# Performance work log

Hardware: AMD Instinct MI355X
Metric: run time of the kernel (lower is better)

## Reference

```python
import jax, jax.numpy as jnp
import numpy as np

EPS = 1e-5

def _ln(x, g, b):
    m = x.mean(-1, keepdims=True)
    v = jnp.var(x, axis=-1, keepdims=True)
    return (x - m) * jax.lax.rsqrt(v + EPS) * g + b

def _conv(x, w, b, stride=1, pad=1):
    y = jax.lax.conv_general_dilated(x, w, (stride, stride), [(pad, pad), (pad, pad)],
                                     dimension_numbers=('NCHW', 'OIHW', 'NCHW'))
    return y + b[None, :, None, None]

def _bn(x, g, b, m, v):
    # inference-mode BatchNorm2d
    inv = jax.lax.rsqrt(v + EPS)
    return (x - m[None, :, None, None]) * (g * inv)[None, :, None, None] + b[None, :, None, None]

def _sru_dir(u0, u1, u2, res, vf, vr, bf, br, reverse):
    # elementwise gated recurrence (SRU v2, identity activation, no dropout)
    def step(c, inp):
        a0, a1, a2, rx = inp
        f = jax.nn.sigmoid(a1 + vf * c + bf)
        c2 = f * c + (1.0 - f) * a0
        r = jax.nn.sigmoid(a2 + vr * c2 + br)
        return c2, r * c2 + (1.0 - r) * rx
    c0 = jnp.zeros_like(u0[0])
    _, hs = jax.lax.scan(step, c0, (u0, u1, u2, res), reverse=reverse)
    return hs

def _sru_layer(x, g, b, wp, w, vc, bias, k, h):
    # x: [L,B,n_in]; layer_norm on input, factored weight (projection), bidirectional
    xn = _ln(x, g, b)
    L, B, _ = xn.shape
    U = (xn @ wp) @ w                      # [L,B,2*k*h]
    U = U.reshape(L, B, 2, k, h)
    outs = []
    for d, rev in ((0, False), (1, True)):
        u = U[:, :, d]
        res = u[..., 3, :] if k == 4 else xn[..., d * h:(d + 1) * h]
        outs.append(_sru_dir(u[..., 0, :], u[..., 1, :], u[..., 2, :], res,
                             vc[d, 0], vc[d, 1], bias[d, 0], bias[d, 1], rev))
    return jnp.concatenate(outs, axis=-1)

def _forward(x, conv0_w, conv0_b, rconv1_w, rconv1_b, rbn1_g, rbn1_b, rbn1_m, rbn1_v,
             rconv2_w, rconv2_b, rbn2_g, rbn2_b, rbn2_m, rbn2_v,
             ln0_g, ln0_b, wproj0, w0, vc0, bias0, ln_g, ln_b, wproj, w, vc, bias,
             cln_g, cln_b, cls_w):
    H = 512
    h = _conv(x, conv0_w, conv0_b, stride=2)           # [B,32,F/2,T/2]
    for i in range(3):                                  # 3 residual blocks
        r = h
        h1 = jax.nn.relu(_bn(_conv(h, rconv1_w[i], rconv1_b[i]), rbn1_g[i], rbn1_b[i], rbn1_m[i], rbn1_v[i]))
        h2 = _bn(_conv(h1, rconv2_w[i], rconv2_b[i]), rbn2_g[i], rbn2_b[i], rbn2_m[i], rbn2_v[i])
        h = jax.nn.relu(h2 + r)
    Bb, C, Fr, Tt = h.shape
    s = h.reshape(Bb, C * Fr, Tt).transpose(2, 0, 1)   # [T,B,2048]
    s = _sru_layer(s, ln0_g, ln0_b, wproj0, w0, vc0, bias0, 4, H)  # layer 0: n_in != n_out -> k=4
    for i in range(3):                                  # layers 1..3: n_in == n_out -> k=3
        s = _sru_layer(s, ln_g[i], ln_b[i], wproj[i], w[i], vc[i], bias[i], 3, H)
    s = s.transpose(1, 0, 2)                            # [B,T,1024]
    s = _ln(s, cln_g, cln_b)
    return s @ cls_w                                    # [B,T,30]

def setup_inputs():
    key = jax.random.key(0)
    ks = iter(jax.random.split(key, 32))
    def nrm(shape, scale=1.0):
        return jax.random.normal(next(ks), shape, jnp.float32) * scale
    H, P, F2, D, hb = 512, 256, 2048, 1024, -2.0
    d = {}
    d['x'] = nrm((16, 1, 128, 2048))
    d['conv0_w'] = nrm((32, 1, 3, 3), (2.0 / 9) ** 0.5)
    d['conv0_b'] = jnp.zeros((32,))
    d['rconv1_w'] = nrm((3, 32, 32, 3, 3), (2.0 / (32 * 9)) ** 0.5)
    d['rconv1_b'] = jnp.zeros((3, 32))
    d['rbn1_g'] = jnp.ones((3, 32)); d['rbn1_b'] = jnp.zeros((3, 32))
    d['rbn1_m'] = nrm((3, 32), 0.1); d['rbn1_v'] = jnp.ones((3, 32))
    d['rconv2_w'] = nrm((3, 32, 32, 3, 3), (2.0 / (32 * 9)) ** 0.5)
    d['rconv2_b'] = jnp.zeros((3, 32))
    d['rbn2_g'] = 0.1 * jnp.ones((3, 32)); d['rbn2_b'] = jnp.zeros((3, 32))
    d['rbn2_m'] = nrm((3, 32), 0.1); d['rbn2_v'] = jnp.ones((3, 32))
    d['ln0_g'] = jnp.ones((F2,)); d['ln0_b'] = jnp.zeros((F2,))
    d['wproj0'] = nrm((F2, P), F2 ** -0.5)
    d['w0'] = nrm((P, 2 * 4 * H), P ** -0.5)
    d['vc0'] = nrm((2, 2, H), 0.1)
    d['bias0'] = jnp.zeros((2, 2, H)).at[:, 0].set(hb)
    d['ln_g'] = jnp.ones((3, D)); d['ln_b'] = jnp.zeros((3, D))
    d['wproj'] = nrm((3, D, P), D ** -0.5)
    d['w'] = nrm((3, P, 2 * 3 * H), P ** -0.5)
    d['vc'] = nrm((3, 2, 2, H), 0.1)
    d['bias'] = jnp.zeros((3, 2, 2, H)).at[:, :, 0].set(hb)
    d['cln_g'] = jnp.ones((D,)); d['cln_b'] = jnp.zeros((D,))
    d['cls_w'] = nrm((D, 30), D ** -0.5)
    return d

def reference(x, conv0_w, conv0_b, rconv1_w, rconv1_b, rbn1_g, rbn1_b, rbn1_m, rbn1_v,
              rconv2_w, rconv2_b, rbn2_g, rbn2_b, rbn2_m, rbn2_v,
              ln0_g, ln0_b, wproj0, w0, vc0, bias0, ln_g, ln_b, wproj, w, vc, bias,
              cln_g, cln_b, cls_w):
    return _forward(x, conv0_w, conv0_b, rconv1_w, rconv1_b, rbn1_g, rbn1_b, rbn1_m, rbn1_v,
                    rconv2_w, rconv2_b, rbn2_g, rbn2_b, rbn2_m, rbn2_v,
                    ln0_g, ln0_b, wproj0, w0, vc0, bias0, ln_g, ln_b, wproj, w, vc, bias,
                    cln_g, cln_b, cls_w)
```

## Files before the change

kernel.cpp:

```cpp
#include <hip/hip_runtime.h>
#include <hip/hip_bf16.h>
#include <math.h>

#define DEV __device__ __forceinline__

typedef __attribute__((ext_vector_type(8))) short short8;
typedef __attribute__((ext_vector_type(4))) float floatx4;

DEV float b2f_lo(unsigned u) { return __uint_as_float(u << 16); }
DEV float b2f_hi(unsigned u) { return __uint_as_float(u & 0xffff0000u); }

#if __has_builtin(__builtin_amdgcn_exp2f)
DEV float fexp2_(float x) { return __builtin_amdgcn_exp2f(x); }
#else
DEV float fexp2_(float x) { return exp2f(x); }
#endif
#if __has_builtin(__builtin_amdgcn_rcpf)
DEV float frcp_(float x) { return __builtin_amdgcn_rcpf(x); }
#else
DEV float frcp_(float x) { return 1.f / x; }
#endif

DEV void gl2lds16(const void* g, void* l) {
  __builtin_amdgcn_global_load_lds(
      (const __attribute__((address_space(1))) unsigned int*)g,
      (__attribute__((address_space(3))) unsigned int*)l, 16, 0, 0);
}

union U8 { uint4 u; __hip_bfloat16 h[8]; };

DEV int swz64(int x)    { return (x & ~63) | ((x & 15) << 2) | ((x >> 4) & 3); }
DEV int invswz64(int x) { return (x & ~63) | ((x & 3) << 4) | ((x >> 2) & 15); }

__global__ __launch_bounds__(256) void conv_stem_nhwc(const float* __restrict__ x,
    const float* __restrict__ w, const float* __restrict__ bias,
    __hip_bfloat16* __restrict__ out) {
  __shared__ float sX[3][2052];
  __shared__ float sW[288];
  __shared__ float sB[32];
  const int tid = threadIdx.x;
  const int f = blockIdx.x, n = blockIdx.y;
  const float* xb = x + (size_t)n * 262144;

  for (int i = tid; i < 1536; i += 256) {
    int r = i >> 9, c4 = i & 511;
    int fi = 2 * f - 1 + r;
    float4 v = {0.f, 0.f, 0.f, 0.f};
    if (fi >= 0 && fi < 128) v = *(const float4*)&xb[fi * 2048 + c4 * 4];
    sX[r][1 + c4 * 4 + 0] = v.x;
    sX[r][1 + c4 * 4 + 1] = v.y;
    sX[r][1 + c4 * 4 + 2] = v.z;
    sX[r][1 + c4 * 4 + 3] = v.w;
  }
  if (tid < 3) { sX[tid][0] = 0.f; sX[tid][2049] = 0.f; }
  for (int i = tid; i < 288; i += 256) sW[i] = w[i];
  if (tid < 32) sB[tid] = bias[tid];
  __syncthreads();

  float xv[4][9];
#pragma unroll
  for (int q = 0; q < 4; ++q) {
    int t = tid + q * 256;
#pragma unroll
    for (int r = 0; r < 3; ++r)
#pragma unroll
      for (int dc = 0; dc < 3; ++dc)
        xv[q][r * 3 + dc] = sX[r][2 * t + dc];
  }

  U8 ores[4][4];
#pragma unroll
  for (int ocq = 0; ocq < 4; ++ocq) {
#pragma unroll
    for (int oo = 0; oo < 8; ++oo) {
      float w9[9];
#pragma unroll
      for (int qq = 0; qq < 9; ++qq) w9[qq] = sW[(ocq * 8 + oo) * 9 + qq];
      float b0 = sB[ocq * 8 + oo];
#pragma unroll
      for (int q = 0; q < 4; ++q) {
        float acc = b0;
#pragma unroll
        for (int qq = 0; qq < 9; ++qq) acc = fmaf(w9[qq], xv[q][qq], acc);
        ores[ocq][q].h[oo] = __float2bfloat16(acc);
      }
    }
  }

#pragma unroll
  for (int q = 0; q < 4; ++q) {
    int t = tid + q * 256;
    uint4* dst = (uint4*)&out[(((size_t)n * 64 + f) * 1024 + t) * 32];
    dst[0] = ores[0][q].u;
    dst[1] = ores[1][q].u;
    dst[2] = ores[2][q].u;
    dst[3] = ores[3][q].u;
  }
}

__global__ __launch_bounds__(256) void wtap_conv6(const float* __restrict__ w1,
    const float* __restrict__ w2, __hip_bfloat16* __restrict__ out) {
  int i = blockIdx.x * 256 + threadIdx.x;
  if (i < 55296) {
    int b = i / 9216, r = i - b * 9216;
    int layer = b >> 1, which = b & 1;
    const float* src = (which ? w2 : w1) + layer * 9216;
    int tap = r >> 10, oc = (r >> 5) & 31, ic = r & 31;
    out[b * 9216 + r] = __float2bfloat16(src[(oc * 32 + ic) * 9 + tap]);
  }
}

template <int ADD>
__global__ __launch_bounds__(256) void conv_mfma(const __hip_bfloat16* __restrict__ Hin,
    const __hip_bfloat16* __restrict__ wt,
    const float* __restrict__ cb, const float* __restrict__ bg,
    const float* __restrict__ bb, const float* __restrict__ bm,
    const float* __restrict__ bv, __hip_bfloat16* Hres) {
  __shared__ __hip_bfloat16 sIn[6 * 66 * 40];
  __hip_bfloat16* sOut = sIn;
  const int tid = threadIdx.x;
  const int tb = blockIdx.x, fb = blockIdx.y, n = blockIdx.z;
  const int t0 = tb * 64, f0 = fb * 4;
  const __hip_bfloat16* Hb = Hin + (size_t)n * 2097152;

  for (int c = tid; c < 1584; c += 256) {
    int rr = c / 264;
    int r2 = c - rr * 264;
    int p = r2 >> 2, icq = r2 & 3;
    int fi = f0 - 1 + rr;
    int tg = t0 + p - 1;
    uint4 v = {0, 0, 0, 0};
    if (fi >= 0 && fi < 64 && tg >= 0 && tg < 1024)
      v = *(const uint4*)&Hb[((size_t)fi * 1024 + tg) * 32 + icq * 8];
    *(uint4*)&sIn[(rr * 66 + p) * 40 + icq * 8] = v;
  }

  const int lane = tid & 63, wave = tid >> 6;
  const int fr = lane & 15, fq = lane >> 4;
  short8 bfrag[9][2];
#pragma unroll
  for (int tap = 0; tap < 9; ++tap)
#pragma unroll
    for (int j = 0; j < 2; ++j)
      bfrag[tap][j] = *(const short8*)&wt[(tap * 32 + j * 16 + fr) * 32 + fq * 8];

  __syncthreads();

  const int tw = wave * 16;
  floatx4 acc[4][2];
#pragma unroll
  for (int fp = 0; fp < 4; ++fp)
#pragma unroll
    for (int j = 0; j < 2; ++j) acc[fp][j] = (floatx4){0.f, 0.f, 0.f, 0.f};

#pragma unroll
  for (int fp = 0; fp < 4; ++fp) {
    int pbase = tw + fr;
#pragma unroll
    for (int df = 0; df < 3; ++df)
#pragma unroll
      for (int dc = 0; dc < 3; ++dc) {
        short8 af =
            *(const short8*)&sIn[((fp + df) * 66 + pbase + dc) * 40 + fq * 8];
        acc[fp][0] = __builtin_amdgcn_mfma_f32_16x16x32_bf16(
            af, bfrag[df * 3 + dc][0], acc[fp][0], 0, 0, 0);
        acc[fp][1] = __builtin_amdgcn_mfma_f32_16x16x32_bf16(
            af, bfrag[df * 3 + dc][1], acc[fp][1], 0, 0, 0);
      }
  }

  float sc0 = bg[fr] * rsqrtf(bv[fr] + 1e-5f);
  float sh0 = (cb[fr] - bm[fr]) * sc0 + bb[fr];
  float sc1 = bg[fr + 16] * rsqrtf(bv[fr + 16] + 1e-5f);
  float sh1 = (cb[fr + 16] - bm[fr + 16]) * sc1 + bb[fr + 16];

  __syncthreads();
#pragma unroll
  for (int fp = 0; fp < 4; ++fp)
#pragma unroll
    for (int j = 0; j < 2; ++j) {
      float sc = j ? sc1 : sc0, sh = j ? sh1 : sh0;
#pragma unroll
      for (int reg = 0; reg < 4; ++reg) {
        int t_l = tw + fq * 4 + reg;
        sOut[(fp * 64 + t_l) * 40 + j * 16 + fr] =
            __float2bfloat16(acc[fp][j][reg] * sc + sh);
      }
    }
  __syncthreads();

  for (int c = tid; c < 1024; c += 256) {
    int fp = c >> 8, rem = c & 255;
    int t_l = rem >> 2, icq = rem & 3;
    U8 y;
    y.u = *(uint4*)&sOut[(fp * 64 + t_l) * 40 + icq * 8];
    size_t addr = (((size_t)n * 64 + f0 + fp) * 1024 + t0 + t_l) * 32 + icq * 8;
    U8 o;
    if (ADD) {
      U8 r;
      r.u = *(const uint4*)&Hres[addr];
#pragma unroll
      for (int i = 0; i < 8; ++i)
        o.h[i] = __float2bfloat16(
            fmaxf(__bfloat162float(y.h[i]) + __bfloat162float(r.h[i]), 0.f));
    } else {
#pragma unroll
      for (int i = 0; i < 8; ++i)
        o.h[i] = __float2bfloat16(fmaxf(__bfloat162float(y.h[i]), 0.f));
    }
    *(uint4*)&Hres[addr] = o.u;
  }
}

__global__ __launch_bounds__(256) void ln_nhwc(const __hip_bfloat16* __restrict__ H,
    const float* __restrict__ g, const float* __restrict__ b,
    __hip_bfloat16* __restrict__ xn) {
  int r = blockIdx.x;
  int t = r >> 4, n = r & 15;
  int tid = threadIdx.x;
  int f = tid >> 2, icq = tid & 3;
  U8 v;
  v.u = *(const uint4*)&H[(((size_t)n * 64 + f) * 1024 + t) * 32 + icq * 8];
  float xv[8];
  float sum = 0.f, ss = 0.f;
#pragma unroll
  for (int i = 0; i < 8; ++i) {
    xv[i] = __bfloat162float(v.h[i]);
    sum += xv[i];
    ss += xv[i] * xv[i];
  }
#pragma unroll
  for (int off = 32; off > 0; off >>= 1) {
    sum += __shfl_down(sum, off);
    ss  += __shfl_down(ss, off);
  }
  __shared__ float red[8];
  int lane = tid & 63, wave = tid >> 6;
  if (lane == 0) { red[wave] = sum; red[4 + wave] = ss; }
  __syncthreads();
  sum = red[0] + red[1] + red[2] + red[3];
  ss  = red[4] + red[5] + red[6] + red[7];
  float mean = sum * (1.f / 2048.f);
  float var = ss * (1.f / 2048.f) - mean * mean;
  float inv = rsqrtf(var + 1e-5f);
  U8 o;
#pragma unroll
  for (int i = 0; i < 8; ++i) {
    int cf = (icq * 8 + i) * 64 + f;
    o.h[i] = __float2bfloat16((xv[i] - mean) * inv * g[cf] + b[cf]);
  }
  *(uint4*)&xn[(size_t)r * 2048 + tid * 8] = o.u;
}

__global__ __launch_bounds__(256) void wt_perm0(const float* __restrict__ in,
    __hip_bfloat16* __restrict__ out) {
  int i = blockIdx.x * 256 + threadIdx.x;
  int p = i >> 11, kp = i & 2047;
  int ic = kp & 31, f = kp >> 5;
  out[i] = __float2bfloat16(in[(ic * 64 + f) * 256 + p]);
}

__global__ __launch_bounds__(256) void wt_bf16(const float* __restrict__ in,
    __hip_bfloat16* __restrict__ out, int K, int N, int inStride, int outStride) {
  __shared__ float tile[32][33];
  int x = threadIdx.x, y0 = threadIdx.y;
  int bn = blockIdx.x * 32;
  int bk = blockIdx.y * 32;
  const float* src = in + (size_t)blockIdx.z * inStride;
  __hip_bfloat16* dst = out + (size_t)blockIdx.z * outStride;
#pragma unroll
  for (int i = 0; i < 4; ++i) {
    int yy = y0 + i * 8;
    tile[yy][x] = src[(size_t)(bk + yy) * N + bn + x];
  }
  __syncthreads();
#pragma unroll
  for (int i = 0; i < 4; ++i) {
    int yy = y0 + i * 8;
    dst[(size_t)(bn + yy) * K + bk + x] = __float2bfloat16(tile[x][yy]);
  }
}

__global__ void wexp_prep(const float* __restrict__ in,
    __hip_bfloat16* __restrict__ out, int korig, int inStride, int outStride) {
  __shared__ float tile[32][33];
  int jt = blockIdx.x;
  int ckt = blockIdx.y;
  int z = blockIdx.z;
  int layer = z >> 3, dk = z & 7;
  int d = dk >> 2, k = dk & 3;
  if (k >= korig) return;
  const float* src = in + (size_t)layer * inStride;
  __hip_bfloat16* dst = out + (size_t)layer * outStride;
  int x = threadIdx.x, y0 = threadIdx.y;
#pragma unroll
  for (int i = 0; i < 4; ++i) {
    int yy = y0 + i * 8;
    tile[yy][x] = src[(size_t)(ckt * 32 + yy) * (korig * 1024) +
                      (d * korig + k) * 512 + jt * 32 + x];
  }
  __syncthreads();
#pragma unroll
  for (int i = 0; i < 4; ++i) {
    int yy = y0 + i * 8;
    int ch = d * 512 + jt * 32 + yy;
    int rOld;
    if (korig == 4)
      rOld = (k < 2) ? (ch * 2 + k) : (2048 + ch * 2 + (k - 2));
    else
      rOld = (k < 2) ? (ch * 2 + k) : (2048 + ch);
    int rNew = invswz64(rOld);
    int ckp = swz64(ckt * 32 + x);
    dst[(size_t)rNew * 256 + ckp] = __float2bfloat16(tile[x][yy]);
  }
}

__global__ __launch_bounds__(256) void colsb_prep(const float* __restrict__ bias0,
    const float* __restrict__ bias3, float2* __restrict__ out) {
  int i = blockIdx.x * 256 + threadIdx.x;
  if (i >= 13312) return;
  const float NL2E = -1.44269504f;
  float s = 1.f, bb = 0.f;
  if (i < 4096) {
    int col = i;
    if (col < 2048) {
      int ch = col >> 1, e = col & 1;
      int d = ch >> 9, jj = ch & 511;
      if (e) { s = NL2E; bb = NL2E * bias0[d * 1024 + jj]; }
    } else {
      int cc = col - 2048, ch = cc >> 1, e = cc & 1;
      int d = ch >> 9, jj = ch & 511;
      if (!e) { s = NL2E; bb = NL2E * bias0[d * 1024 + 512 + jj]; }
    }
  } else {
    int rem = i - 4096;
    int layer = rem / 3072, col = rem - layer * 3072;
    const float* bsrc = bias3 + layer * 2048;
    if (col < 2048) {
      int ch = col >> 1, e = col & 1;
      int d = ch >> 9, jj = ch & 511;
      if (e) { s = NL2E; bb = NL2E * bsrc[d * 1024 + jj]; }
    } else {
      int ch = col - 2048;
      int d = ch >> 9, jj = ch & 511;
      s = NL2E; bb = NL2E * bsrc[d * 1024 + 512 + jj];
    }
  }
  out[i] = make_float2(s, bb);
}

__global__ __launch_bounds__(256) void wct_prep(const float* __restrict__ in,
    __hip_bfloat16* __restrict__ out) {
  int i = blockIdx.x * 256 + threadIdx.x;
  int nn = i >> 10, kk = i & 1023;
  out[i] = __float2bfloat16(nn < 30 ? in[kk * 30 + nn] : 0.f);
}

__global__ __launch_bounds__(256) void gemm_bf16(const __hip_bfloat16* __restrict__ A,
    const __hip_bfloat16* __restrict__ Bt, __hip_bfloat16* __restrict__ C,
    const float2* __restrict__ csb, int M, int N, int K) {
  __shared__ __hip_bfloat16 As[2][128 * 64];
  __shared__ __hip_bfloat16 Bs[2][128 * 64];
  const int tid = threadIdx.x;
  const int gx = gridDim.x;
  const int nwg = gx * gridDim.y;
  const int bid = blockIdx.y * gx + blockIdx.x;
  const int wgid = (bid & 7) * (nwg >> 3) + (bid >> 3);
  const int m0 = (wgid / gx) * 128, n0 = (wgid % gx) * 128;
  const int lane = tid & 63, wave = tid >> 6;
  const int wm = wave & 1, wn = wave >> 1;
  const int fr = lane & 15, fq = lane >> 4;
  const int frx = fr & 7;

  const int srow8 = lane >> 3;
  const int lslot = (lane & 7) ^ srow8;
  const __hip_bfloat16* gaS = &A[(size_t)(m0 + wave * 32 + srow8) * K + lslot * 8];
  const __hip_bfloat16* gbS = &Bt[(size_t)(n0 + wave * 32 + srow8) * K + lslot * 8];

  floatx4 acc[4][4];
#pragma unroll
  for (int i = 0; i < 4; ++i)
#pragma unroll
    for (int j = 0; j < 4; ++j)
      acc[i][j] = (floatx4){0.f, 0.f, 0.f, 0.f};

#define STAGE(BUF, kk)                                                    \
  {                                                                       \
    _Pragma("unroll") for (int i = 0; i < 4; ++i) {                       \
      gl2lds16(gaS + (size_t)i * 8 * K + (kk),                            \
               &As[BUF][(wave * 32 + i * 8) * 64]);                       \
      gl2lds16(gbS + (size_t)i * 8 * K + (kk),                            \
               &Bs[BUF][(wave * 32 + i * 8) * 64]);                       \
    }                                                                     \
  }
#define COMPUTE(BUF)                                                      \
  {                                                                       \
    _Pragma("unroll") for (int s = 0; s < 2; ++s) {                       \
      const int sl = ((s * 4 + fq) ^ frx) * 8;                            \
      short8 af[4], bf_[4];                                               \
      _Pragma("unroll") for (int i = 0; i < 4; ++i) {                     \
        af[i]  = *(const short8*)&As[BUF][(wm * 64 + i * 16 + fr) * 64 + sl]; \
        bf_[i] = *(const short8*)&Bs[BUF][(wn * 64 + i * 16 + fr) * 64 + sl]; \
      }                                                                   \
      _Pragma("unroll") for (int i = 0; i < 4; ++i)                       \
        _Pragma("unroll") for (int j = 0; j < 4; ++j)                     \
          acc[i][j] = __builtin_amdgcn_mfma_f32_16x16x32_bf16(            \
              af[i], bf_[j], acc[i][j], 0, 0, 0);                         \
    }                                                                     \
  }
#define CFENCE asm volatile("" ::: "memory")

  STAGE(0, 0);
  for (int k0 = 0; k0 < K; k0 += 128) {
    STAGE(1, k0 + 64);
    asm volatile("s_waitcnt vmcnt(8)" ::: "memory");
    __builtin_amdgcn_s_barrier();
    COMPUTE(0);
    CFENCE;
    __builtin_amdgcn_s_barrier();
    if (k0 + 128 < K) {
      STAGE(0, k0 + 128);
      asm volatile("s_waitcnt vmcnt(8)" ::: "memory");
    } else {
      asm volatile("s_waitcnt vmcnt(0)" ::: "memory");
    }
    __builtin_amdgcn_s_barrier();
    COMPUTE(1);
    CFENCE;
    __builtin_amdgcn_s_barrier();
  }
#undef STAGE
#undef COMPUTE
#undef CFENCE

  const int p0 = n0 + wn * 64 + fr * 4;
  float s0 = 1.f, s1 = 1.f, s2 = 1.f, s3 = 1.f;
  float c0 = 0.f, c1 = 0.f, c2v = 0.f, c3 = 0.f;
  if (csb) {
    float2 t0 = csb[p0], t1 = csb[p0 + 1], t2 = csb[p0 + 2], t3 = csb[p0 + 3];
    s0 = t0.x; c0 = t0.y; s1 = t1.x; c1 = t1.y;
    s2 = t2.x; c2v = t2.y; s3 = t3.x; c3 = t3.y;
  }
#pragma unroll
  for (int i = 0; i < 4; ++i)
#pragma unroll
    for (int reg = 0; reg < 4; ++reg) {
      int row = m0 + wm * 64 + i * 16 + fq * 4 + reg;
      union { uint2 u; __hip_bfloat16 h[4]; } o;
      o.h[0] = __float2bfloat16(fmaf(acc[i][0][reg], s0, c0));
      o.h[1] = __float2bfloat16(fmaf(acc[i][1][reg], s1, c1));
      o.h[2] = __float2bfloat16(fmaf(acc[i][2][reg], s2, c2v));
      o.h[3] = __float2bfloat16(fmaf(acc[i][3][reg], s3, c3));
      *(uint2*)&C[(size_t)row * N + p0] = o.u;
    }
}

__global__ __launch_bounds__(256) void cls_gemm(const __hip_bfloat16* __restrict__ A,
    const __hip_bfloat16* __restrict__ Wct, float* __restrict__ out) {
  const int tid = threadIdx.x;
  const int lane = tid & 63, wave = tid >> 6;
  const int fr = lane & 15, fq = lane >> 4;
  const int m0 = (blockIdx.x * 4 + wave) * 16;
  floatx4 acc[2];
  acc[0] = (floatx4){0.f, 0.f, 0.f, 0.f};
  acc[1] = (floatx4){0.f, 0.f, 0.f, 0.f};
#pragma unroll 4
  for (int k0 = 0; k0 < 1024; k0 += 32) {
    short8 af = *(const short8*)&A[(size_t)(m0 + fr) * 1024 + k0 + fq * 8];
    short8 b0 = *(const short8*)&Wct[(size_t)fr * 1024 + k0 + fq * 8];
    short8 b1 = *(const short8*)&Wct[(size_t)(16 + fr) * 1024 + k0 + fq * 8];
    acc[0] = __builtin_amdgcn_mfma_f32_16x16x32_bf16(af, b0, acc[0], 0, 0, 0);
    acc[1] = __builtin_amdgcn_mfma_f32_16x16x32_bf16(af, b1, acc[1], 0, 0, 0);
  }
#pragma unroll
  for (int j = 0; j < 2; ++j) {
    int col = j * 16 + fr;
    if (col < 30) {
#pragma unroll
      for (int reg = 0; reg < 4; ++reg) {
        int row = m0 + fq * 4 + reg;
        int t = row >> 4, n = row & 15;
        out[(size_t)n * 30720 + t * 30 + col] = acc[j][reg];
      }
    }
  }
}

template <int ROWB>
__global__ __launch_bounds__(64) void scan_c(const __hip_bfloat16* __restrict__ U,
    const float* __restrict__ vc, __hip_bfloat16* __restrict__ c2out) {
  int gid = blockIdx.x * 64 + threadIdx.x;
  int j = gid & 511;
  int n = (gid >> 9) & 15;
  int d = gid >> 13;
  const float NL2E = -1.44269504f;
  float vf2 = NL2E * vc[d * 1024 + j];

  const char* Ub = (const char*)U + (size_t)n * ROWB + (size_t)(d * 512 + j) * 4;
  char* Ob = (char*)c2out + (size_t)n * 2048 + (size_t)(d * 512 + j) * 2;
  const int US = d ? -(16 * ROWB) : (16 * ROWB);
  const int OS = d ? -32768 : 32768;
  int uoff = d ? 1023 * 16 * ROWB : 0;
  int ooff = d ? 1023 * 32768 : 0;

  uint B0[16], B1[16], B2[16], B3[16];
  float c = 0.f;

#define LOADC(UB)                                                         \
  {                                                                       \
    _Pragma("unroll") for (int ss = 0; ss < 16; ++ss) {                   \
      UB[ss] = *(const uint*)(Ub + uoff);                                 \
      uoff += US;                                                         \
    }                                                                     \
  }

#define COMPC(UB)                                                         \
  {                                                                       \
    _Pragma("unroll") for (int ss = 0; ss < 16; ++ss) {                   \
      uint u = UB[ss];                                                    \
      float a0 = b2f_lo(u), a1p = b2f_hi(u);                              \
      float f = frcp_(1.f + fexp2_(fmaf(vf2, c, a1p)));                   \
      c = fmaf(f, c - a0, a0);                                            \
      *(__hip_bfloat16*)(Ob + ooff) = __float2bfloat16(c);                \
      ooff += OS;                                                         \
    }                                                                     \
  }

  LOADC(B0);
  LOADC(B1);
  LOADC(B2);
  for (int cb = 0; cb < 64; cb += 4) {
    LOADC(B3);
    COMPC(B0);
    if (cb + 4 < 64) LOADC(B0);
    COMPC(B1);
    if (cb + 5 < 64) LOADC(B1);
    COMPC(B2);
    if (cb + 6 < 64) LOADC(B2);
    COMPC(B3);
  }
#undef LOADC
#undef COMPC
}

template <int K4>
__global__ __launch_bounds__(256) void yln(const __hip_bfloat16* __restrict__ c2buf,
    const __hip_bfloat16* __restrict__ U, const __hip_bfloat16* __restrict__ xn,
    const float* __restrict__ vc, const float* __restrict__ g,
    const float* __restrict__ b, __hip_bfloat16* __restrict__ outx) {
  int r = blockIdx.x;
  int tid = threadIdx.x;
  int ch0 = tid * 4;
  const float NL2E = -1.44269504f;

  union { ushort4 u; __hip_bfloat16 h[4]; } cv;
  cv.u = *(const ushort4*)&c2buf[(size_t)r * 1024 + ch0];
  float a2p[4], rx[4];
  if (K4) {
    uint4 pr = *(const uint4*)((const char*)U + (size_t)r * 8192 + 4096 + tid * 16);
    uint pp[4] = {pr.x, pr.y, pr.z, pr.w};
#pragma unroll
    for (int i = 0; i < 4; ++i) { a2p[i] = b2f_lo(pp[i]); rx[i] = b2f_hi(pp[i]); }
  } else {
    union { ushort4 u; __hip_bfloat16 h[4]; } av, xv;
    av.u = *(const ushort4*)((const char*)U + (size_t)r * 6144 + 4096 + tid * 8);
    xv.u = *(const ushort4*)&xn[(size_t)r * 1024 + ch0];
#pragma unroll
    for (int i = 0; i < 4; ++i) {
      a2p[i] = __bfloat162float(av.h[i]);
      rx[i]  = __bfloat162float(xv.h[i]);
    }
  }

  int d = ch0 >> 9, j0 = ch0 & 511;
  float y[4], sum = 0.f, ss = 0.f;
#pragma unroll
  for (int i = 0; i < 4; ++i) {
    float vr2 = NL2E * vc[d * 1024 + 512 + j0 + i];
    float cc = __bfloat162float(cv.h[i]);
    float rr = frcp_(1.f + fexp2_(fmaf(vr2, cc, a2p[i])));
    y[i] = fmaf(rr, cc - rx[i], rx[i]);
    sum += y[i];
    ss += y[i] * y[i];
  }
#pragma unroll
  for (int off = 32; off > 0; off >>= 1) {
    sum += __shfl_down(sum, off);
    ss  += __shfl_down(ss, off);
  }
  __shared__ float red[8];
  int lane = tid & 63, wave = tid >> 6;
  if (lane == 0) { red[wave] = sum; red[4 + wave] = ss; }
  __syncthreads();
  sum = red[0] + red[1] + red[2] + red[3];
  ss  = red[4] + red[5] + red[6] + red[7];
  float mean = sum * (1.f / 1024.f);
  float var = ss * (1.f / 1024.f) - mean * mean;
  float inv = rsqrtf(var + 1e-5f);
  float4 gv = *(const float4*)&g[ch0];
  float4 bv = *(const float4*)&b[ch0];
  float gg[4] = {gv.x, gv.y, gv.z, gv.w};
  float bb[4] = {bv.x, bv.y, bv.z, bv.w};
  union { ushort4 u; __hip_bfloat16 h[4]; } o;
#pragma unroll
  for (int i = 0; i < 4; ++i)
    o.h[i] = __float2bfloat16((y[i] - mean) * inv * gg[i] + bb[i]);
  *(ushort4*)&outx[(size_t)r * 1024 + ch0] = o.u;
}

extern "C" void kernel_launch(void* const* d_in, const int* in_sizes, int n_in,
                              void* d_out, int out_size, void* d_ws, size_t ws_size,
                              hipStream_t stream) {
  const float* x        = (const float*)d_in[0];
  const float* conv0_w  = (const float*)d_in[1];
  const float* conv0_b  = (const float*)d_in[2];
  const float* rconv1_w = (const float*)d_in[3];
  const float* rconv1_b = (const float*)d_in[4];
  const float* rbn1_g   = (const float*)d_in[5];
  const float* rbn1_b   = (const float*)d_in[6];
  const float* rbn1_m   = (const float*)d_in[7];
  const float* rbn1_v   = (const float*)d_in[8];
  const float* rconv2_w = (const float*)d_in[9];
  const float* rconv2_b = (const float*)d_in[10];
  const float* rbn2_g   = (const float*)d_in[11];
  const float* rbn2_b   = (const float*)d_in[12];
  const float* rbn2_m   = (const float*)d_in[13];
  const float* rbn2_v   = (const float*)d_in[14];
  const float* ln0_g    = (const float*)d_in[15];
  const float* ln0_b    = (const float*)d_in[16];
  const float* wproj0   = (const float*)d_in[17];
  const float* w0       = (const float*)d_in[18];
  const float* vc0      = (const float*)d_in[19];
  const float* bias0    = (const float*)d_in[20];
  const float* ln_g     = (const float*)d_in[21];
  const float* ln_b     = (const float*)d_in[22];
  const float* wproj    = (const float*)d_in[23];
  const float* w        = (const float*)d_in[24];
  const float* vc       = (const float*)d_in[25];
  const float* bias     = (const float*)d_in[26];
  const float* cln_g    = (const float*)d_in[27];
  const float* cln_b    = (const float*)d_in[28];
  const float* cls_w    = (const float*)d_in[29];
  float* out = (float*)d_out;

  float* Af = (float*)d_ws;
  float* Bf = Af + 33554432;
  __hip_bfloat16* Ah = (__hip_bfloat16*)Af;
  __hip_bfloat16* Bh = (__hip_bfloat16*)Bf;

  __hip_bfloat16* hA     = Ah;
  __hip_bfloat16* hB     = Bh;
  __hip_bfloat16* wt_all = Ah + 62914560;
  __hip_bfloat16* Wp0t   = Ah + 52428800;

  __hip_bfloat16* c2   = Bh;
  __hip_bfloat16* xnc  = Bh + 16777216;
  __hip_bfloat16* xn3  = Bh + 33554432;
  __hip_bfloat16* tmp  = Bh + 50331648;
  __hip_bfloat16* W3p  = Bh + 54525952;
  __hip_bfloat16* W0p  = Bh + 57671680;
  __hip_bfloat16* Wpt3 = Bh + 58720256;
  float2* csb          = (float2*)(Bh + 59506688);
  __hip_bfloat16* xn0  = Bh;
  __hip_bfloat16* U    = Ah;
  __hip_bfloat16* Wct  = Ah;

  const float2* csb4 = csb;
  const float2* csb3 = csb + 4096;

  wtap_conv6<<<216, 256, 0, stream>>>(rconv1_w, rconv2_w, wt_all);
  wt_perm0<<<2048, 256, 0, stream>>>(wproj0, Wp0t);
  wexp_prep<<<dim3(16, 8, 8), dim3(32, 8), 0, stream>>>(w0, W0p, 4, 0, 0);
  wexp_prep<<<dim3(16, 8, 24), dim3(32, 8), 0, stream>>>(w, W3p, 3,
                                                         786432, 786432);
  wt_bf16<<<dim3(8, 32, 3), dim3(32, 8), 0, stream>>>(wproj, Wpt3, 1024, 256,
                                                      262144, 262144);
  colsb_prep<<<52, 256, 0, stream>>>(bias0, bias, csb);

  conv_stem_nhwc<<<dim3(64, 16), 256, 0, stream>>>(x, conv0_w, conv0_b, hA);
  for (int i = 0; i < 3; ++i) {
    conv_mfma<0><<<dim3(16, 16, 16), 256, 0, stream>>>(hA, wt_all + (i * 2) * 9216,
        rconv1_b + i * 32, rbn1_g + i * 32, rbn1_b + i * 32,
        rbn1_m + i * 32, rbn1_v + i * 32, hB);
    conv_mfma<1><<<dim3(16, 16, 16), 256, 0, stream>>>(hB, wt_all + (i * 2 + 1) * 9216,
        rconv2_b + i * 32, rbn2_g + i * 32, rbn2_b + i * 32,
        rbn2_m + i * 32, rbn2_v + i * 32, hA);
  }

  ln_nhwc<<<16384, 256, 0, stream>>>(hA, ln0_g, ln0_b, xn0);
  gemm_bf16<<<dim3(2, 128), 256, 0, stream>>>(xn0, Wp0t, tmp, nullptr,
                                              16384, 256, 2048);
  gemm_bf16<<<dim3(32, 128), 256, 0, stream>>>(tmp, W0p, U, csb4,
                                               16384, 4096, 256);
  scan_c<8192><<<256, 64, 0, stream>>>(U, vc0, c2);
  __hip_bfloat16* xnA = xn3;
  __hip_bfloat16* xnB = xnc;
  yln<1><<<16384, 256, 0, stream>>>(c2, U, nullptr, vc0, ln_g, ln_b, xnA);

  for (int i = 0; i < 3; ++i) {
    gemm_bf16<<<dim3(2, 128), 256, 0, stream>>>(xnA, Wpt3 + i * 262144, tmp,
                                                nullptr, 16384, 256, 1024);
    gemm_bf16<<<dim3(24, 128), 256, 0, stream>>>(tmp, W3p + i * 786432, U,
                                                 csb3 + i * 3072, 16384, 3072, 256);
    scan_c<6144><<<256, 64, 0, stream>>>(U, vc + i * 2048, c2);
    const float* gg = (i < 2) ? (ln_g + (i + 1) * 1024) : cln_g;
    const float* bb = (i < 2) ? (ln_b + (i + 1) * 1024) : cln_b;
    yln<0><<<16384, 256, 0, stream>>>(c2, U, xnA, vc + i * 2048, gg, bb, xnB);
    __hip_bfloat16* sw = xnA; xnA = xnB; xnB = sw;
  }

  wct_prep<<<128, 256, 0, stream>>>(cls_w, Wct);
  cls_gemm<<<256, 256, 0, stream>>>(xnA, Wct, out);
}
```

Measured before the change: 974.7 us.

## Split GEMM epilogue into time-major scan buffer and separate gate/residual buffer

The second projection GEMM now writes its output in two layouts. The (a0,a1) pairs go to a channel-major buffer where each channel's 16 batch elements are contiguous per timestep. The remaining columns go to a compact separate buffer. The scan kernel is remapped so each 16-lane group reads one channel across 16 batch entries contiguously, making its strided serial loads coalesced. yln reads the smaller compact buffer. The cost is a more scattered store pattern in the GEMM epilogue.

```diff
diff --git a/kernel.cpp b/kernel.cpp
--- a/kernel.cpp
+++ b/kernel.cpp
@@ -356,8 +356,10 @@
   out[i] = __float2bfloat16(nn < 30 ? in[kk * 30 + nn] : 0.f);
 }
 
+template <int SPLIT>
 __global__ __launch_bounds__(256) void gemm_bf16(const __hip_bfloat16* __restrict__ A,
     const __hip_bfloat16* __restrict__ Bt, __hip_bfloat16* __restrict__ C,
+    uint* __restrict__ U01, __hip_bfloat16* __restrict__ U23,
     const float2* __restrict__ csb, int M, int N, int K) {
   __shared__ __hip_bfloat16 As[2][128 * 64];
   __shared__ __hip_bfloat16 Bs[2][128 * 64];
@@ -441,18 +443,56 @@
     s0 = t0.x; c0 = t0.y; s1 = t1.x; c1 = t1.y;
     s2 = t2.x; c2v = t2.y; s3 = t3.x; c3 = t3.y;
   }
-#pragma unroll
-  for (int i = 0; i < 4; ++i)
-#pragma unroll
-    for (int reg = 0; reg < 4; ++reg) {
-      int row = m0 + wm * 64 + i * 16 + fq * 4 + reg;
-      union { uint2 u; __hip_bfloat16 h[4]; } o;
-      o.h[0] = __float2bfloat16(fmaf(acc[i][0][reg], s0, c0));
-      o.h[1] = __float2bfloat16(fmaf(acc[i][1][reg], s1, c1));
-      o.h[2] = __float2bfloat16(fmaf(acc[i][2][reg], s2, c2v));
-      o.h[3] = __float2bfloat16(fmaf(acc[i][3][reg], s3, c3));
-      *(uint2*)&C[(size_t)row * N + p0] = o.u;
-    }
+
+  if (SPLIT == 0) {
+#pragma unroll
+    for (int i = 0; i < 4; ++i)
+#pragma unroll
+      for (int reg = 0; reg < 4; ++reg) {
+        int row = m0 + wm * 64 + i * 16 + fq * 4 + reg;
+        union { uint2 u; __hip_bfloat16 h[4]; } o;
+        o.h[0] = __float2bfloat16(fmaf(acc[i][0][reg], s0, c0));
+        o.h[1] = __float2bfloat16(fmaf(acc[i][1][reg], s1, c1));
+        o.h[2] = __float2bfloat16(fmaf(acc[i][2][reg], s2, c2v));
+        o.h[3] = __float2bfloat16(fmaf(acc[i][3][reg], s3, c3));
+        *(uint2*)&C[(size_t)row * N + p0] = o.u;
+      }
+  } else if (p0 < 2048) {
+    const int cell0 = p0 >> 1;
+    uint4* ub = (uint4*)U01;
+#pragma unroll
+    for (int i = 0; i < 4; ++i) {
+      int t = (m0 + wm * 64 + i * 16) >> 4;
+      union { uint4 u; __hip_bfloat16 h[8]; } q0, q1;
+#pragma unroll
+      for (int reg = 0; reg < 4; ++reg) {
+        q0.h[reg * 2]     = __float2bfloat16(fmaf(acc[i][0][reg], s0, c0));
+        q0.h[reg * 2 + 1] = __float2bfloat16(fmaf(acc[i][1][reg], s1, c1));
+        q1.h[reg * 2]     = __float2bfloat16(fmaf(acc[i][2][reg], s2, c2v));
+        q1.h[reg * 2 + 1] = __float2bfloat16(fmaf(acc[i][3][reg], s3, c3));
+      }
+      ub[((size_t)cell0 * 1024 + t) * 4 + fq] = q0.u;
+      ub[((size_t)(cell0 + 1) * 1024 + t) * 4 + fq] = q1.u;
+    }
+  } else {
+    const int cc = p0 - 2048;
+#pragma unroll
+    for (int i = 0; i < 4; ++i)
+#pragma unroll
+      for (int reg = 0; reg < 4; ++reg) {
+        int row = m0 + wm * 64 + i * 16 + fq * 4 + reg;
+        union { uint2 u; __hip_bfloat16 h[4]; } o;
+        o.h[0] = __float2bfloat16(fmaf(acc[i][0][reg], s0, c0));
+        o.h[1] = __float2bfloat16(fmaf(acc[i][1][reg], s1, c1));
+        o.h[2] = __float2bfloat16(fmaf(acc[i][2][reg], s2, c2v));
+        o.h[3] = __float2bfloat16(fmaf(acc[i][3][reg], s3, c3));
+        if (SPLIT == 1) {
+          *(uint2*)&((uint*)U23)[(size_t)row * 1024 + (cc >> 1)] = o.u;
+        } else {
+          *(uint2*)&U23[(size_t)row * 1024 + cc] = o.u;
+        }
+      }
+  }
 }
 
 __global__ __launch_bounds__(256) void cls_gemm(const __hip_bfloat16* __restrict__ A,
@@ -486,21 +526,21 @@
   }
 }
 
-template <int ROWB>
-__global__ __launch_bounds__(64) void scan_c(const __hip_bfloat16* __restrict__ U,
+__global__ __launch_bounds__(64) void scan_c(const uint* __restrict__ U01,
     const float* __restrict__ vc, __hip_bfloat16* __restrict__ c2out) {
-  int gid = blockIdx.x * 64 + threadIdx.x;
-  int j = gid & 511;
-  int n = (gid >> 9) & 15;
-  int d = gid >> 13;
+  int b = blockIdx.x;
+  int lane = threadIdx.x;
+  int ch = (b & 31) * 32 + (b >> 5) * 4 + (lane >> 4);
+  int n = lane & 15;
+  int d = ch >> 9;
   const float NL2E = -1.44269504f;
-  float vf2 = NL2E * vc[d * 1024 + j];
-
-  const char* Ub = (const char*)U + (size_t)n * ROWB + (size_t)(d * 512 + j) * 4;
-  char* Ob = (char*)c2out + (size_t)n * 2048 + (size_t)(d * 512 + j) * 2;
-  const int US = d ? -(16 * ROWB) : (16 * ROWB);
+  float vf2 = NL2E * vc[d * 1024 + (ch & 511)];
+
+  const uint* Up = U01 + (size_t)ch * 16384 + n;
+  char* Ob = (char*)c2out + ((size_t)n * 1024 + ch) * 2;
+  const int US = d ? -16 : 16;
   const int OS = d ? -32768 : 32768;
-  int uoff = d ? 1023 * 16 * ROWB : 0;
+  int uoff = d ? 1023 * 16 : 0;
   int ooff = d ? 1023 * 32768 : 0;
 
   uint B0[16], B1[16], B2[16], B3[16];
@@ -509,7 +549,7 @@
 #define LOADC(UB)                                                         \
   {                                                                       \
     _Pragma("unroll") for (int ss = 0; ss < 16; ++ss) {                   \
-      UB[ss] = *(const uint*)(Ub + uoff);                                 \
+      UB[ss] = Up[uoff];                                                  \
       uoff += US;                                                         \
     }                                                                     \
   }
@@ -545,7 +585,7 @@
 
 template <int K4>
 __global__ __launch_bounds__(256) void yln(const __hip_bfloat16* __restrict__ c2buf,
-    const __hip_bfloat16* __restrict__ U, const __hip_bfloat16* __restrict__ xn,
+    const __hip_bfloat16* __restrict__ U23, const __hip_bfloat16* __restrict__ xn,
     const float* __restrict__ vc, const float* __restrict__ g,
     const float* __restrict__ b, __hip_bfloat16* __restrict__ outx) {
   int r = blockIdx.x;
@@ -557,13 +597,13 @@
   cv.u = *(const ushort4*)&c2buf[(size_t)r * 1024 + ch0];
   float a2p[4], rx[4];
   if (K4) {
-    uint4 pr = *(const uint4*)((const char*)U + (size_t)r * 8192 + 4096 + tid * 16);
+    uint4 pr = *(const uint4*)((const char*)U23 + (size_t)r * 4096 + tid * 16);
     uint pp[4] = {pr.x, pr.y, pr.z, pr.w};
 #pragma unroll
     for (int i = 0; i < 4; ++i) { a2p[i] = b2f_lo(pp[i]); rx[i] = b2f_hi(pp[i]); }
   } else {
     union { ushort4 u; __hip_bfloat16 h[4]; } av, xv;
-    av.u = *(const ushort4*)((const char*)U + (size_t)r * 6144 + 4096 + tid * 8);
+    av.u = *(const ushort4*)((const char*)U23 + (size_t)r * 2048 + tid * 8);
     xv.u = *(const ushort4*)&xn[(size_t)r * 1024 + ch0];
 #pragma unroll
     for (int i = 0; i < 4; ++i) {
@@ -653,6 +693,10 @@
   __hip_bfloat16* wt_all = Ah + 62914560;
   __hip_bfloat16* Wp0t   = Ah + 52428800;
 
+  uint* U01            = (uint*)Ah;
+  __hip_bfloat16* U23  = Ah + 33554432;
+  __hip_bfloat16* Wct  = Ah;
+
   __hip_bfloat16* c2   = Bh;
   __hip_bfloat16* xnc  = Bh + 16777216;
   __hip_bfloat16* xn3  = Bh + 33554432;
@@ -662,8 +706,6 @@
   __hip_bfloat16* Wpt3 = Bh + 58720256;
   float2* csb          = (float2*)(Bh + 59506688);
   __hip_bfloat16* xn0  = Bh;
-  __hip_bfloat16* U    = Ah;
-  __hip_bfloat16* Wct  = Ah;
 
   const float2* csb4 = csb;
   const float2* csb3 = csb + 4096;
@@ -688,24 +730,26 @@
   }
 
   ln_nhwc<<<16384, 256, 0, stream>>>(hA, ln0_g, ln0_b, xn0);
-  gemm_bf16<<<dim3(2, 128), 256, 0, stream>>>(xn0, Wp0t, tmp, nullptr,
-                                              16384, 256, 2048);
-  gemm_bf16<<<dim3(32, 128), 256, 0, stream>>>(tmp, W0p, U, csb4,
-                                               16384, 4096, 256);
-  scan_c<8192><<<256, 64, 0, stream>>>(U, vc0, c2);
+  gemm_bf16<0><<<dim3(2, 128), 256, 0, stream>>>(xn0, Wp0t, tmp, nullptr, nullptr,
+                                                 nullptr, 16384, 256, 2048);
+  gemm_bf16<1><<<dim3(32, 128), 256, 0, stream>>>(tmp, W0p, nullptr, U01, U23,
+                                                  csb4, 16384, 4096, 256);
+  scan_c<<<256, 64, 0, stream>>>(U01, vc0, c2);
   __hip_bfloat16* xnA = xn3;
   __hip_bfloat16* xnB = xnc;
-  yln<1><<<16384, 256, 0, stream>>>(c2, U, nullptr, vc0, ln_g, ln_b, xnA);
+  yln<1><<<16384, 256, 0, stream>>>(c2, U23, nullptr, vc0, ln_g, ln_b, xnA);
 
   for (int i = 0; i < 3; ++i) {
-    gemm_bf16<<<dim3(2, 128), 256, 0, stream>>>(xnA, Wpt3 + i * 262144, tmp,
-                                                nullptr, 16384, 256, 1024);
-    gemm_bf16<<<dim3(24, 128), 256, 0, stream>>>(tmp, W3p + i * 786432, U,
-                                                 csb3 + i * 3072, 16384, 3072, 256);
-    scan_c<6144><<<256, 64, 0, stream>>>(U, vc + i * 2048, c2);
+    gemm_bf16<0><<<dim3(2, 128), 256, 0, stream>>>(xnA, Wpt3 + i * 262144, tmp,
+                                                   nullptr, nullptr, nullptr,
+                                                   16384, 256, 1024);
+    gemm_bf16<2><<<dim3(24, 128), 256, 0, stream>>>(tmp, W3p + i * 786432, nullptr,
+                                                    U01, U23, csb3 + i * 3072,
+                                                    16384, 3072, 256);
+    scan_c<<<256, 64, 0, stream>>>(U01, vc + i * 2048, c2);
     const float* gg = (i < 2) ? (ln_g + (i + 1) * 1024) : cln_g;
     const float* bb = (i < 2) ? (ln_b + (i + 1) * 1024) : cln_b;
-    yln<0><<<16384, 256, 0, stream>>>(c2, U, xnA, vc + i * 2048, gg, bb, xnB);
+    yln<0><<<16384, 256, 0, stream>>>(c2, U23, xnA, vc + i * 2048, gg, bb, xnB);
     __hip_bfloat16* sw = xnA; xnA = xnB; xnB = sw;
   }
 
```

After: 1.010 ms. 3.6% more time.

## Warp-specialize SRU scan with a producer wave streaming U into an LDS ring

Applied to the files above, without the earlier changes.

The recurrent scan kernel now uses two waves per block. One producer wave issues async global-to-LDS loads of U into a 16-slot ring buffer, staying 12 blocks ahead of the consumer. The consumer wave reads gate inputs from LDS and runs the recurrence, with the two waves synchronised by block barriers. The aim is to hide global memory latency on the serial scan better than the register-based prefetch did, at the cost of 64KB of LDS per block and a barrier on every 16-step chunk.

```diff
diff --git a/kernel.cpp b/kernel.cpp
--- a/kernel.cpp
+++ b/kernel.cpp
@@ -487,60 +487,68 @@
 }
 
 template <int ROWB>
-__global__ __launch_bounds__(64) void scan_c(const __hip_bfloat16* __restrict__ U,
+__global__ __launch_bounds__(128) void scan_c(const __hip_bfloat16* __restrict__ U,
     const float* __restrict__ vc, __hip_bfloat16* __restrict__ c2out) {
-  int gid = blockIdx.x * 64 + threadIdx.x;
-  int j = gid & 511;
-  int n = (gid >> 9) & 15;
-  int d = gid >> 13;
+  __shared__ uint slab[16 * 1024];
+  const int b = blockIdx.x;
+  const int lane = threadIdx.x & 63;
+  const int wave = threadIdx.x >> 6;
+  const int jb = (b * 64) & 511;
+  const int n = (b >> 3) & 15;
+  const int d = b >> 7;
   const float NL2E = -1.44269504f;
-  float vf2 = NL2E * vc[d * 1024 + j];
-
-  const char* Ub = (const char*)U + (size_t)n * ROWB + (size_t)(d * 512 + j) * 4;
-  char* Ob = (char*)c2out + (size_t)n * 2048 + (size_t)(d * 512 + j) * 2;
-  const int US = d ? -(16 * ROWB) : (16 * ROWB);
-  const int OS = d ? -32768 : 32768;
-  int uoff = d ? 1023 * 16 * ROWB : 0;
-  int ooff = d ? 1023 * 32768 : 0;
-
-  uint B0[16], B1[16], B2[16], B3[16];
-  float c = 0.f;
-
-#define LOADC(UB)                                                         \
-  {                                                                       \
-    _Pragma("unroll") for (int ss = 0; ss < 16; ++ss) {                   \
-      UB[ss] = *(const uint*)(Ub + uoff);                                 \
-      uoff += US;                                                         \
-    }                                                                     \
-  }
-
-#define COMPC(UB)                                                         \
-  {                                                                       \
-    _Pragma("unroll") for (int ss = 0; ss < 16; ++ss) {                   \
-      uint u = UB[ss];                                                    \
-      float a0 = b2f_lo(u), a1p = b2f_hi(u);                              \
-      float f = frcp_(1.f + fexp2_(fmaf(vf2, c, a1p)));                   \
-      c = fmaf(f, c - a0, a0);                                            \
-      *(__hip_bfloat16*)(Ob + ooff) = __float2bfloat16(c);                \
-      ooff += OS;                                                         \
-    }                                                                     \
-  }
-
-  LOADC(B0);
-  LOADC(B1);
-  LOADC(B2);
-  for (int cb = 0; cb < 64; cb += 4) {
-    LOADC(B3);
-    COMPC(B0);
-    if (cb + 4 < 64) LOADC(B0);
-    COMPC(B1);
-    if (cb + 5 < 64) LOADC(B1);
-    COMPC(B2);
-    if (cb + 6 < 64) LOADC(B2);
-    COMPC(B3);
-  }
-#undef LOADC
-#undef COMPC
+
+  const ptrdiff_t US = (ptrdiff_t)16 * ROWB;
+  const char* stripe0 = (const char*)U + (size_t)n * ROWB + (size_t)(d * 512 + jb) * 4;
+  const char* baseDir = d ? stripe0 + 1023 * US : stripe0;
+  const ptrdiff_t stepStride = d ? -US : US;
+
+  if (wave == 1) {
+    const int D = 12;
+    const int sgrp = lane >> 4;
+    const int chunk = lane & 15;
+#define ISSUE4(BB)                                                        \
+    {                                                                     \
+      int slot = (BB) & 15;                                               \
+      _Pragma("unroll") for (int i = 0; i < 4; ++i) {                     \
+        int s = (BB) * 16 + i * 4 + sgrp;                                 \
+        const char* src = baseDir + (ptrdiff_t)s * stepStride + chunk * 16; \
+        gl2lds16(src, (char*)slab + slot * 4096 + i * 1024);              \
+      }                                                                   \
+    }
+    for (int bb = 0; bb < D; ++bb) ISSUE4(bb);
+    for (int bb = 0; bb < 64; ++bb) {
+      if (bb + D < 64) {
+        ISSUE4(bb + D);
+        asm volatile("s_waitcnt vmcnt(48)" ::: "memory");
+      } else {
+        asm volatile("s_waitcnt vmcnt(0)" ::: "memory");
+      }
+      __builtin_amdgcn_s_barrier();
+    }
+#undef ISSUE4
+  } else {
+    const int j = jb + lane;
+    float vf2 = NL2E * vc[d * 1024 + j];
+    char* Ob = (char*)c2out + (size_t)n * 2048 + (size_t)(d * 512 + j) * 2;
+    const int OS = d ? -32768 : 32768;
+    int ooff = d ? 1023 * 32768 : 0;
+    float c = 0.f;
+    for (int bb = 0; bb < 64; ++bb) {
+      __builtin_amdgcn_s_barrier();
+      asm volatile("" ::: "memory");
+      const uint* slot = slab + (bb & 15) * 1024;
+#pragma unroll
+      for (int ss = 0; ss < 16; ++ss) {
+        uint u = slot[ss * 64 + lane];
+        float a0 = b2f_lo(u), a1p = b2f_hi(u);
+        float f = frcp_(1.f + fexp2_(fmaf(vf2, c, a1p)));
+        c = fmaf(f, c - a0, a0);
+        *(__hip_bfloat16*)(Ob + ooff) = __float2bfloat16(c);
+        ooff += OS;
+      }
+    }
+  }
 }
 
 template <int K4>
@@ -692,7 +700,7 @@
                                               16384, 256, 2048);
   gemm_bf16<<<dim3(32, 128), 256, 0, stream>>>(tmp, W0p, U, csb4,
                                                16384, 4096, 256);
-  scan_c<8192><<<256, 64, 0, stream>>>(U, vc0, c2);
+  scan_c<8192><<<256, 128, 0, stream>>>(U, vc0, c2);
   __hip_bfloat16* xnA = xn3;
   __hip_bfloat16* xnB = xnc;
   yln<1><<<16384, 256, 0, stream>>>(c2, U, nullptr, vc0, ln_g, ln_b, xnA);
@@ -702,7 +710,7 @@
                                                 nullptr, 16384, 256, 1024);
     gemm_bf16<<<dim3(24, 128), 256, 0, stream>>>(tmp, W3p + i * 786432, U,
                                                  csb3 + i * 3072, 16384, 3072, 256);
-    scan_c<6144><<<256, 64, 0, stream>>>(U, vc + i * 2048, c2);
+    scan_c<6144><<<256, 128, 0, stream>>>(U, vc + i * 2048, c2);
     const float* gg = (i < 2) ? (ln_g + (i + 1) * 1024) : cln_g;
     const float* bb = (i < 2) ? (ln_b + (i + 1) * 1024) : cln_b;
     yln<0><<<16384, 256, 0, stream>>>(c2, U, xnA, vc + i * 2048, gg, bb, xnB);
```

After: 966.1 us (median of 2 runs). About the same (-0.9%).
